# Optimization experiments

Measured on AMD Instinct MI355X. Metric: run time of the kernel, lower is better.

The kernel has to match this reference:

```python
import jax, jax.numpy as jnp
import numpy as np

B, H, W = 4, 1024, 1024

# 8-tap Sobel-style stencil: offsets in (u, v) units of (dx, dy)
OFF_U = jnp.array([-1.0, -1.0, -1.0, 0.0, 0.0, 1.0, 1.0, 1.0], dtype=jnp.float32)
OFF_V = jnp.array([-1.0, 0.0, 1.0, -1.0, 1.0, -1.0, 0.0, 1.0], dtype=jnp.float32)
KU = jnp.array([-0.25, -0.5, -0.25, 0.0, 0.0, 0.25, 0.5, 0.25], dtype=jnp.float32)
KV = jnp.array([-0.25, 0.0, 0.25, -0.5, 0.5, -0.25, 0.0, 0.25], dtype=jnp.float32)


def setup_inputs() -> dict:
    key = jax.random.key(0)
    k1, k2 = jax.random.split(key)
    x = jax.random.uniform(k1, (B, 3, H, W), dtype=jnp.float32)
    sigma = jax.random.uniform(k2, (B,), dtype=jnp.float32) * 2.0 + 0.5  # pixels
    return {"x": x, "sigma": sigma}


def _bilinear(tex, u, v):
    # tex: [3, H, W]; u, v: [8, H, W] normalized UV in [0,1]
    Hh, Ww = tex.shape[1], tex.shape[2]
    px = u * Ww - 0.5
    py = v * Hh - 0.5
    x0 = jnp.floor(px)
    y0 = jnp.floor(py)
    fx = (px - x0)[None]  # [1,8,H,W]
    fy = (py - y0)[None]
    x0i = jnp.clip(x0.astype(jnp.int32), 0, Ww - 1)
    x1i = jnp.clip(x0i + 1, 0, Ww - 1)
    y0i = jnp.clip(y0.astype(jnp.int32), 0, Hh - 1)
    y1i = jnp.clip(y0i + 1, 0, Hh - 1)
    t00 = tex[:, y0i, x0i]  # [3,8,H,W]
    t01 = tex[:, y0i, x1i]
    t10 = tex[:, y1i, x0i]
    t11 = tex[:, y1i, x1i]
    return (t00 * (1 - fx) * (1 - fy) + t01 * fx * (1 - fy)
            + t10 * (1 - fx) * fy + t11 * fx * fy)


def reference(x, sigma):
    Bb, C, Hh, Ww = x.shape
    ys, xs = jnp.meshgrid(jnp.arange(Hh, dtype=x.dtype),
                          jnp.arange(Ww, dtype=x.dtype), indexing='ij')
    u0 = (xs + 0.5) / Ww  # pixel-center UV
    v0 = (ys + 0.5) / Hh
    dx = sigma / Ww  # [B]
    dy = sigma / Hh
    u = u0[None, None] + OFF_U[None, :, None, None] * dx[:, None, None, None]  # [B,8,H,W]
    v = v0[None, None] + OFF_V[None, :, None, None] * dy[:, None, None, None]
    s = jax.vmap(_bilinear)(x, u, v)  # [B,3,8,H,W]
    s_u = jnp.einsum('bcthw,t->bchw', s, KU)
    s_v = jnp.einsum('bcthw,t->bchw', s, KV)
    lum = jnp.array([100.0, 1.0, 1.0], dtype=x.dtype)[None, :, None, None]
    s_u = s_u * lum
    s_v = s_v * lum
    # structure tensor components E, G, F
    return jnp.stack([(s_u * s_u).sum(1), (s_v * s_v).sum(1), (s_u * s_v).sum(1)], axis=1)
```

## Files before the change

### kernel.cpp

```cpp
#include <hip/hip_runtime.h>


#define W_ 1024
#define H_ 1024
#define PLANE (1 << 20)
#define TCOLS 64
#define TROWS 32
#define ROWS 8
#define LSTRIDE 72

__device__ __forceinline__ float lerp1(float a, float b, float f) {
    return fmaf(f, b - a, a);
}

__device__ void slow_pixel(const float* __restrict__ Xb, float* __restrict__ Ob,
                           float sg, int xi, int y)
{
    float imf = floorf(-sg), ipf = floorf(sg);
    float fm  = -sg - imf;
    float fp  =  sg - ipf;
    int   im  = (int)imf, ip = (int)ipf;

    int cm0 = min(max(xi + im, 0), W_ - 1), cm1 = min(cm0 + 1, W_ - 1);
    int cp0 = min(max(xi + ip, 0), W_ - 1), cp1 = min(cp0 + 1, W_ - 1);
    int rm0 = min(max(y + im, 0), H_ - 1),  rm1 = min(rm0 + 1, H_ - 1);
    int rp0 = min(max(y + ip, 0), H_ - 1),  rp1 = min(rp0 + 1, H_ - 1);

    int o_rm0 = rm0 << 10, o_rm1 = rm1 << 10;
    int o_rp0 = rp0 << 10, o_rp1 = rp1 << 10;
    int o_r0  = y   << 10;

    float oxx = 0.f, oyy = 0.f, oxy = 0.f;

    #pragma unroll
    for (int c = 0; c < 3; ++c) {
        const float* base = Xb + ((size_t)c << 20);

        float hm_m0 = lerp1(base[o_rm0 + cm0], base[o_rm0 + cm1], fm);
        float hm_m1 = lerp1(base[o_rm1 + cm0], base[o_rm1 + cm1], fm);
        float hm_0  = lerp1(base[o_r0  + cm0], base[o_r0  + cm1], fm);
        float hm_p0 = lerp1(base[o_rp0 + cm0], base[o_rp0 + cm1], fm);
        float hm_p1 = lerp1(base[o_rp1 + cm0], base[o_rp1 + cm1], fm);
        float hp_m0 = lerp1(base[o_rm0 + cp0], base[o_rm0 + cp1], fp);
        float hp_m1 = lerp1(base[o_rm1 + cp0], base[o_rm1 + cp1], fp);
        float hp_0  = lerp1(base[o_r0  + cp0], base[o_r0  + cp1], fp);
        float hp_p0 = lerp1(base[o_rp0 + cp0], base[o_rp0 + cp1], fp);
        float hp_p1 = lerp1(base[o_rp1 + cp0], base[o_rp1 + cp1], fp);
        float h0_m0 = base[o_rm0 + xi], h0_m1 = base[o_rm1 + xi];
        float h0_p0 = base[o_rp0 + xi], h0_p1 = base[o_rp1 + xi];

        float t0 = lerp1(hm_m0, hm_m1, fm);
        float t1 = hm_0;
        float t2 = lerp1(hm_p0, hm_p1, fp);
        float t3 = lerp1(h0_m0, h0_m1, fm);
        float t4 = lerp1(h0_p0, h0_p1, fp);
        float t5 = lerp1(hp_m0, hp_m1, fm);
        float t6 = hp_0;
        float t7 = lerp1(hp_p0, hp_p1, fp);

        float su = 0.25f * (t5 + t7 - t0 - t2) + 0.5f * (t6 - t1);
        float sv = 0.25f * (t2 + t7 - t0 - t5) + 0.5f * (t4 - t3);

        float l2 = (c == 0) ? 10000.f : 1.f;
        oxx = fmaf(l2 * su, su, oxx);
        oyy = fmaf(l2 * sv, sv, oyy);
        oxy = fmaf(l2 * su, sv, oxy);
    }

    int pix = (y << 10) | xi;
    Ob[pix]             = oxx;
    Ob[PLANE + pix]     = oyy;
    Ob[2 * PLANE + pix] = oxy;
}

template<int N>
__device__ __forceinline__ void acc(float (&arr)[N], int k, float val) {
    if (k >= 0 && k < N) arr[k] += val;
}

template<int IP>
__device__ void fast_tile(const float* __restrict__ Xb, float* __restrict__ Ob,
                          float fp, float fm, int x0, int y0,
                          int tx, int ty, int tid, float* smem)
{
    constexpr int LROWS = TROWS + 2 * IP + 2;
    constexpr int RW    = ROWS + 2 * IP + 2;
    constexpr int NG    = LROWS * 18;

    int x = x0 + tx;
    int Y = y0 + ty * ROWS;

    float oxx[ROWS], oyy[ROWS], oxy[ROWS];
    #pragma unroll
    for (int k = 0; k < ROWS; ++k) { oxx[k] = 0.f; oyy[k] = 0.f; oxy[k] = 0.f; }

    const float* sp = smem + (ty * ROWS) * LSTRIDE + tx + (3 - IP);

    for (int c = 0; c < 3; ++c) {
        const float* Xc = Xb + ((size_t)c << 20);

        for (int g = tid; g < NG; g += 256) {
            int row = g / 18;
            int grp = g - row * 18;
            int gr  = min(max(y0 - IP - 1 + row, 0), H_ - 1);
            int gc  = min(max(x0 - 4 + grp * 4, 0), W_ - 4);
            *reinterpret_cast<float4*>(&smem[row * LSTRIDE + grp * 4]) =
                *reinterpret_cast<const float4*>(&Xc[(gr << 10) + gc]);
        }
        __syncthreads();

        float su[ROWS], sv[ROWS];
        #pragma unroll
        for (int k = 0; k < ROWS; ++k) { su[k] = 0.f; sv[k] = 0.f; }

        #pragma unroll
        for (int w = 0; w < RW; ++w) {
            float a0 = sp[w * LSTRIDE];
            float a1 = sp[w * LSTRIDE + 1];
            float cc = sp[w * LSTRIDE + IP + 1];
            float b0 = sp[w * LSTRIDE + 2 * IP + 1];
            float b1 = sp[w * LSTRIDE + 2 * IP + 2];
            float hm = lerp1(a0, a1, fm);
            float hp = lerp1(b0, b1, fp);
            float q  = hp - hm;
            float A  = 0.25f * q;
            float hq = 0.5f  * q;
            float Bv = fmaf(0.25f, hm + hp, 0.5f * cc);
            float fpA = fp * A,  fmA = fm * A;
            float fpB = fp * Bv, fmB = fm * Bv;

            acc(su, w,              fpA);
            acc(su, w - 1,          fmA);
            acc(su, w - IP - 1,     hq);
            acc(su, w - 2*IP - 1,   fmA);
            acc(su, w - 2*IP - 2,   fpA);
            acc(sv, w,             -fpB);
            acc(sv, w - 1,         -fmB);
            acc(sv, w - 2*IP - 1,   fmB);
            acc(sv, w - 2*IP - 2,   fpB);
        }

        float l2 = (c == 0) ? 10000.f : 1.f;
        #pragma unroll
        for (int k = 0; k < ROWS; ++k) {
            oxx[k] = fmaf(l2 * su[k], su[k], oxx[k]);
            oyy[k] = fmaf(l2 * sv[k], sv[k], oyy[k]);
            oxy[k] = fmaf(l2 * su[k], sv[k], oxy[k]);
        }
        __syncthreads();
    }

    bool okx = (x > IP) && (x < W_ - 1 - IP);
    #pragma unroll
    for (int k = 0; k < ROWS; ++k) {
        int y = Y + k;
        if (okx && y > IP) {
            int pix = (y << 10) | x;
            Ob[pix]             = oxx[k];
            Ob[PLANE + pix]     = oyy[k];
            Ob[2 * PLANE + pix] = oxy[k];
        }
    }
}

__global__ __launch_bounds__(256) void st_kernel(
    const float* __restrict__ X, const float* __restrict__ S,
    float* __restrict__ O)
{
    int b  = blockIdx.z;
    const float* Xb = X + (size_t)b * 3 * PLANE;
    float*       Ob = O + (size_t)b * 3 * PLANE;
    float sg = S[b];

    int tx = threadIdx.x, ty = threadIdx.y;
    int tid = ty * 64 + tx;

    if (blockIdx.y == (H_ / TROWS)) {
        int t = blockIdx.x * 256 + tid;
        #pragma unroll
        for (int it = 0; it < 3; ++it) {
            int pidx = t + it * 4096;
            if (pidx < 6144) {
                int yy = pidx / 6;
                int cc = pidx - yy * 6;
                int xx = (cc < 3) ? cc : (W_ - 6 + cc);
                slow_pixel(Xb, Ob, sg, xx, yy);
            } else if (pidx < 9216) {
                int p2 = pidx - 6144;
                slow_pixel(Xb, Ob, sg, p2 & 1023, p2 >> 10);
            }
        }
        return;
    }

    int x0 = blockIdx.x * TCOLS;
    int y0 = blockIdx.y * TROWS;

    int ipv = (int)floorf(sg);
    int imv = (int)floorf(-sg);
    bool sig_ok = (imv == -ipv - 1) && ipv >= 0 && ipv <= 2;
    float fp = sg - (float)ipv;
    float fm = 1.0f - fp;

    __shared__ float smem[(TROWS + 6) * LSTRIDE];

    if (sig_ok) {
        switch (ipv) {
            case 0:  fast_tile<0>(Xb, Ob, fp, fm, x0, y0, tx, ty, tid, smem); break;
            case 1:  fast_tile<1>(Xb, Ob, fp, fm, x0, y0, tx, ty, tid, smem); break;
            default: fast_tile<2>(Xb, Ob, fp, fm, x0, y0, tx, ty, tid, smem); break;
        }
    } else {
        for (int k = 0; k < ROWS; ++k)
            slow_pixel(Xb, Ob, sg, x0 + tx, y0 + ty * ROWS + k);
    }
}

extern "C" void kernel_launch(void* const* d_in, const int* in_sizes, int n_in,
                              void* d_out, int out_size, void* d_ws, size_t ws_size,
                              hipStream_t stream) {
    const float* x     = (const float*)d_in[0];
    const float* sigma = (const float*)d_in[1];
    float* out = (float*)d_out;

    dim3 grid(W_ / TCOLS, H_ / TROWS + 1, 4), block(64, 4);
    hipLaunchKernelGGL(st_kernel, grid, block, 0, stream, x, sigma, out);
}
```

Baseline: 117.4 us.

## Stage all three channels into LDS at once via direct global-to-LDS loads

Replaces the per-channel cooperative float4 load and its two barriers with a single up-front staging of all three channel tiles into LDS. The staging uses the global_load_lds builtin, so data goes from global memory to LDS without passing through registers. Loads for every channel can then be in flight together, and two of the three sync pairs are removed. The cost is a threefold larger LDS footprint per block, which may reduce occupancy. Correctness depends on the LDS addressing and async-completion rules of the builtin.

```diff
diff --git a/kernel.cpp b/kernel.cpp
--- a/kernel.cpp
+++ b/kernel.cpp
@@ -11,6 +11,13 @@
 
 __device__ __forceinline__ float lerp1(float a, float b, float f) {
     return fmaf(f, b - a, a);
+}
+
+__device__ __forceinline__ void async_copy16(const float* g, float* s) {
+    __builtin_amdgcn_global_load_lds(
+        (const __attribute__((address_space(1))) unsigned int*)g,
+        (__attribute__((address_space(3))) unsigned int*)s,
+        16, 0, 0);
 }
 
 __device__ void slow_pixel(const float* __restrict__ Xb, float* __restrict__ Ob,
@@ -83,31 +90,42 @@
                           float fp, float fm, int x0, int y0,
                           int tx, int ty, int tid, float* smem)
 {
-    constexpr int LROWS = TROWS + 2 * IP + 2;
-    constexpr int RW    = ROWS + 2 * IP + 2;
-    constexpr int NG    = LROWS * 18;
+    constexpr int LROWS  = TROWS + 2 * IP + 2;
+    constexpr int RW     = ROWS + 2 * IP + 2;
+    constexpr int NG     = 3 * LROWS * 18;
+    constexpr int FULLIT = NG / 256;
 
     int x = x0 + tx;
     int Y = y0 + ty * ROWS;
 
+    auto stage = [&](int g) {
+        int row  = g / 18;
+        int grp  = g - row * 18;
+        int c    = row / LROWS;
+        int lrow = row - c * LROWS;
+        int gr   = min(max(y0 - IP - 1 + lrow, 0), H_ - 1);
+        int gc   = min(max(x0 - 4 + grp * 4, 0), W_ - 4);
+        async_copy16(Xb + ((size_t)c << 20) + (gr << 10) + gc,
+                     smem + g * 4);
+    };
+
+    #pragma unroll
+    for (int it = 0; it < FULLIT; ++it)
+        stage(it * 256 + tid);
+    if (FULLIT * 256 + tid < NG)
+        stage(FULLIT * 256 + tid);
+
+    __syncthreads();
+
     float oxx[ROWS], oyy[ROWS], oxy[ROWS];
     #pragma unroll
     for (int k = 0; k < ROWS; ++k) { oxx[k] = 0.f; oyy[k] = 0.f; oxy[k] = 0.f; }
 
-    const float* sp = smem + (ty * ROWS) * LSTRIDE + tx + (3 - IP);
-
+    const float* spb = smem + (ty * ROWS) * LSTRIDE + tx + (3 - IP);
+
+    #pragma unroll
     for (int c = 0; c < 3; ++c) {
-        const float* Xc = Xb + ((size_t)c << 20);
-
-        for (int g = tid; g < NG; g += 256) {
-            int row = g / 18;
-            int grp = g - row * 18;
-            int gr  = min(max(y0 - IP - 1 + row, 0), H_ - 1);
-            int gc  = min(max(x0 - 4 + grp * 4, 0), W_ - 4);
-            *reinterpret_cast<float4*>(&smem[row * LSTRIDE + grp * 4]) =
-                *reinterpret_cast<const float4*>(&Xc[(gr << 10) + gc]);
-        }
-        __syncthreads();
+        const float* sp = spb + c * (LROWS * LSTRIDE);
 
         float su[ROWS], sv[ROWS];
         #pragma unroll
@@ -147,7 +165,6 @@
             oyy[k] = fmaf(l2 * sv[k], sv[k], oyy[k]);
             oxy[k] = fmaf(l2 * su[k], sv[k], oxy[k]);
         }
-        __syncthreads();
     }
 
     bool okx = (x > IP) && (x < W_ - 1 - IP);
@@ -202,7 +219,7 @@
     float fp = sg - (float)ipv;
     float fm = 1.0f - fp;
 
-    __shared__ float smem[(TROWS + 6) * LSTRIDE];
+    __shared__ float smem[3 * (TROWS + 6) * LSTRIDE];
 
     if (sig_ok) {
         switch (ipv) {
```

Measured after the change: 115.3 us. About the same (-1.8%).
